# Performance work log

Hardware: AMD Instinct MI355X
Metric: run time of the kernel (lower is better)

## Reference

```python
import jax, jax.numpy as jnp
import numpy as np
from jax.ops import segment_sum, segment_max

N_NODES = 100000
N_EDGES = 1600000


def _glorot(key, shape):
    fan_in, fan_out = shape[0], shape[-1]
    lim = np.sqrt(6.0 / (fan_in + fan_out))
    return jax.random.uniform(key, shape, jnp.float32, -lim, lim)


def setup_inputs() -> dict:
    key = jax.random.key(0)
    ks = jax.random.split(key, 12)
    x = jax.random.normal(ks[0], (N_NODES, 7), jnp.float32)
    edge_index = jax.random.randint(ks[1], (2, N_EDGES), 0, N_NODES, jnp.int64)
    return {
        "x": x,
        "edge_index": edge_index,
        # GCNConv(7, 32)
        "W1": _glorot(ks[2], (7, 32)), "b1": jnp.zeros((32,), jnp.float32),
        # GATConv(32, 64), heads=1
        "W2": _glorot(ks[3], (32, 64)), "a_src2": _glorot(ks[4], (64, 1))[:, 0],
        "a_dst2": _glorot(ks[5], (64, 1))[:, 0], "b2": jnp.zeros((64,), jnp.float32),
        # GCNConv(64, 128)
        "W3": _glorot(ks[6], (64, 128)), "b3": jnp.zeros((128,), jnp.float32),
        # GATConv(128, 2), heads=1
        "W4": _glorot(ks[7], (128, 2)), "a_src4": _glorot(ks[8], (2, 1))[:, 0],
        "a_dst4": _glorot(ks[9], (2, 1))[:, 0], "b4": jnp.zeros((2,), jnp.float32),
    }


def _gcn_conv(x, src, dst, W, b):
    # x' = W x; symmetric normalization with self-loops already in (src, dst)
    h = x @ W
    deg = segment_sum(jnp.ones_like(dst, dtype=h.dtype), dst, num_segments=N_NODES)
    dinv = jnp.where(deg > 0, jax.lax.rsqrt(deg), 0.0)
    norm = dinv[src] * dinv[dst]            # [E]
    msg = norm[:, None] * h[src]            # [E, C]
    return segment_sum(msg, dst, num_segments=N_NODES) + b


def _gat_conv(x, src, dst, W, a_src, a_dst, b, slope=0.2):
    h = x @ W                               # [N, C]
    alpha_src = h @ a_src                   # [N]
    alpha_dst = h @ a_dst                   # [N]
    e = alpha_src[src] + alpha_dst[dst]     # [E]
    e = jnp.where(e > 0, e, slope * e)      # leaky_relu
    # numerically-stable softmax over edges grouped by destination node
    m = segment_max(e, dst, num_segments=N_NODES)
    ex = jnp.exp(e - m[dst])
    denom = segment_sum(ex, dst, num_segments=N_NODES)
    w = ex / (denom[dst] + 1e-16)           # [E]
    out = segment_sum(w[:, None] * h[src], dst, num_segments=N_NODES)
    return out + b


def reference(x, edge_index, W1, b1, W2, a_src2, a_dst2, b2, W3, b3, W4, a_src4, a_dst4, b4):
    # add self-loops once (PyG does it per layer; identical edge set each time)
    loop = jnp.arange(N_NODES, dtype=edge_index.dtype)
    src = jnp.concatenate([edge_index[0], loop])
    dst = jnp.concatenate([edge_index[1], loop])

    h = _gcn_conv(x, src, dst, W1, b1)
    h = jax.nn.relu(h)
    h = _gat_conv(h, src, dst, W2, a_src2, a_dst2, b2)
    h = jax.nn.relu(h)
    h = _gcn_conv(h, src, dst, W3, b3)
    h = jax.nn.relu(h)
    h = _gat_conv(h, src, dst, W4, a_src4, a_dst4, b4)
    return jax.nn.log_softmax(h, axis=1)
```

## Files before the change

### kernel.cpp

```cpp
#include <hip/hip_runtime.h>
#include <hip/hip_bf16.h>

#define NN 100000
#define NE 1600000
#define NT (NN + NE)
#define NBKT 256
#define BSZ 391
#define BCAP 10240

typedef unsigned int u32;
typedef unsigned short u16;

static __device__ __forceinline__ int clampN(int s) {
    return ((unsigned)s < (unsigned)NN) ? s : 0;
}
static __device__ __forceinline__ int ld_src(const int* ei, int is32, int e) {
    return is32 ? ei[e] : ei[2 * e];
}
static __device__ __forceinline__ int ld_dst(const int* ei, int is32, int e) {
    return is32 ? ei[NE + e] : ei[2 * NE + 2 * e];
}
static __device__ __forceinline__ float2 b2x2(u32 u) {
    float2 r;
    r.x = __uint_as_float((u & 0xffffu) << 16);
    r.y = __uint_as_float(u & 0xffff0000u);
    return r;
}
static __device__ __forceinline__ u16 f2bs(float f) {
    union { __hip_bfloat16 b; u16 u; } cv;
    cv.b = __float2bfloat16(f);
    return cv.u;
}
static __device__ __forceinline__ u32 pack2(float x, float y) {
    return ((u32)f2bs(y) << 16) | (u32)f2bs(x);
}
static __device__ __forceinline__ float lrelu_c(float e) {
    e = (e > 0.f) ? e : 0.2f * e;
    return fminf(e, 60.f);
}

#define FMA4(acc, s, v) { acc.x += (s)*(v).x; acc.y += (s)*(v).y; \
                          acc.z += (s)*(v).z; acc.w += (s)*(v).w; }


__global__ void __launch_bounds__(256) k_init(const float* __restrict__ W2,
                                              const float* __restrict__ a2s,
                                              const float* __restrict__ a2d,
                                              const int* __restrict__ ei,
                                              float* __restrict__ va2,
                                              float* __restrict__ vd2,
                                              int* __restrict__ flag,
                                              int* __restrict__ gcur) {
    if (blockIdx.x == 0) {
        if (threadIdx.x == 0) flag[0] = 0;
        __syncthreads();
        int nz = 0;
        for (int i = threadIdx.x; i < 4096; i += 256) nz |= ei[2 * i + 1];
        if (nz) atomicOr(flag, 1);
        if (threadIdx.x < NBKT) gcur[threadIdx.x] = 0;
    } else if (threadIdx.x < 64) {
        int t = threadIdx.x;
        if (t < 32) {
            float a = 0.f;
            for (int c = 0; c < 64; c++) a += W2[t * 64 + c] * a2s[c];
            va2[t] = a;
        } else {
            int k = t - 32;
            float a = 0.f;
            for (int c = 0; c < 64; c++) a += W2[k * 64 + c] * a2d[c];
            vd2[k] = a;
        }
    }
}


__global__ void __launch_bounds__(256) k_binA(const int* __restrict__ ei,
                                              const int* __restrict__ flag,
                                              int* __restrict__ gcur,
                                              u32* __restrict__ staging) {
    __shared__ int hist[NBKT];
    __shared__ int gbase[NBKT];
    __shared__ int cnt2[NBKT];
    int tid = threadIdx.x;
    if (tid < NBKT) hist[tid] = 0;
    __syncthreads();

    int base = blockIdx.x * 4096;
    int is32 = flag[0];
    int d[16], s[16];
    #pragma unroll
    for (int i = 0; i < 16; i++) {
        int e = base + i * 256 + tid;
        d[i] = -1;
        if (e < NE) {
            int dd = ld_dst(ei, is32, e);
            if ((unsigned)dd < (unsigned)NN) { d[i] = dd; s[i] = clampN(ld_src(ei, is32, e)); }
        } else if (e < NT) {
            d[i] = e - NE; s[i] = e - NE;
        }
        if (d[i] >= 0) atomicAdd(&hist[d[i] / BSZ], 1);
    }
    __syncthreads();
    if (tid < NBKT) {
        int c = hist[tid];
        gbase[tid] = c ? atomicAdd(&gcur[tid], c) : 0;
        cnt2[tid] = 0;
    }
    __syncthreads();
    #pragma unroll
    for (int i = 0; i < 16; i++) {
        if (d[i] >= 0) {
            int b = d[i] / BSZ;
            int pos = gbase[b] + atomicAdd(&cnt2[b], 1);
            if (pos < BCAP)
                staging[(size_t)b * BCAP + pos] =
                    ((unsigned)(d[i] - b * BSZ) << 17) | (unsigned)s[i];
        }
    }
}

__global__ void __launch_bounds__(256) k_histscan(const u32* __restrict__ staging,
                                                  const int* __restrict__ gcur,
                                                  const float* __restrict__ x,
                                                  u32* __restrict__ xpb,
                                                  int* __restrict__ rowptr,
                                                  int* __restrict__ deg,
                                                  int* __restrict__ part) {
    __shared__ int h[512];
    __shared__ int sm[256];
    int b = blockIdx.x, tid = threadIdx.x;
    h[tid] = 0; h[tid + 256] = 0;
    __syncthreads();
    int cnt = min(gcur[b], BCAP);
    const u32* st = staging + (size_t)b * BCAP;
    for (int i = tid; i < cnt; i += 256)
        atomicAdd(&h[st[i] >> 17], 1);
    __syncthreads();
    int h0 = h[2 * tid], h1 = h[2 * tid + 1];
    int pair = h0 + h1;
    sm[tid] = pair;
    __syncthreads();
    for (int off = 1; off < 256; off <<= 1) {
        int t = (tid >= off) ? sm[tid - off] : 0;
        __syncthreads();
        sm[tid] += t;
        __syncthreads();
    }
    int excl = sm[tid] - pair;
    int g0 = b * BSZ + 2 * tid;
    if (2 * tid < BSZ && g0 < NN) { rowptr[g0] = excl; deg[g0] = h0; }
    int g1 = g0 + 1;
    if (2 * tid + 1 < BSZ && g1 < NN) { rowptr[g1] = excl + h0; deg[g1] = h1; }
    if (tid == 255) part[b] = sm[255];

    for (int i = b * 256 + tid; i < NN * 4; i += NBKT * 256) {
        int n = i >> 2, c2 = i & 3;
        float f0 = x[n * 7 + 2 * c2];
        float f1 = (2 * c2 + 1 < 7) ? x[n * 7 + 2 * c2 + 1] : 0.f;
        xpb[i] = pack2(f0, f1);
    }
}

__global__ void __launch_bounds__(256) k_scat(const u32* __restrict__ staging,
                                              const int* __restrict__ gcur,
                                              const int* __restrict__ part,
                                              int* __restrict__ rowptr,
                                              const int* __restrict__ deg,
                                              float* __restrict__ dinv,
                                              int* __restrict__ col) {
    __shared__ int sm[256];
    __shared__ int cur[BSZ];
    int b = blockIdx.x, tid = threadIdx.x;
    int v = part[tid];
    sm[tid] = v;
    __syncthreads();
    for (int off = 1; off < 256; off <<= 1) {
        int t = (tid >= off) ? sm[tid - off] : 0;
        __syncthreads();
        sm[tid] += t;
        __syncthreads();
    }
    int pb = (b > 0) ? sm[b - 1] : 0;
    if (b == 0 && tid == 0) rowptr[NN] = NT;
    for (int l = tid; l < BSZ; l += 256) {
        int g = b * BSZ + l;
        if (g < NN) {
            int r = rowptr[g] + pb;
            rowptr[g] = r;
            cur[l] = r;
            int d = deg[g];
            dinv[g] = rsqrtf((float)(d > 0 ? d : 1));
        } else cur[l] = 0;
    }
    __syncthreads();
    int cnt = min(gcur[b], BCAP);
    const u32* st = staging + (size_t)b * BCAP;
    for (int i = tid; i < cnt; i += 256) {
        u32 w = st[i];
        int l = w >> 17;
        int s = w & 0x1FFFF;
        int p = atomicAdd(&cur[l], 1);
        if ((unsigned)p < (unsigned)NT) col[p] = s;
    }
}


__global__ void __launch_bounds__(256) k_l1(const u32* __restrict__ xpb,
                                            const int* __restrict__ rowptr,
                                            const int* __restrict__ col,
                                            const float* __restrict__ dinv,
                                            const float* __restrict__ W1,
                                            const float* __restrict__ b1,
                                            const float* __restrict__ va2,
                                            const float* __restrict__ vd2,
                                            u32* __restrict__ O1b,
                                            float* __restrict__ as_,
                                            float* __restrict__ ad_) {
    __shared__ float sW1[7 * 32];
    __shared__ float sb1[32], sva[32], svd[32];
    __shared__ float sT1[64 * 8];
    if (threadIdx.x < 224) sW1[threadIdx.x] = W1[threadIdx.x];
    else {
        int c = threadIdx.x - 224;
        sb1[c] = b1[c]; sva[c] = va2[c]; svd[c] = vd2[c];
    }
    __syncthreads();

    int node_l = threadIdx.x >> 2;
    int lane = threadIdx.x & 3;
    int slot = lane >> 1;
    int ck = lane & 1;
    int n = blockIdx.x * 64 + node_l;
    if (n >= NN) return;
    {
        int beg = rowptr[n], end = rowptr[n + 1];
        float a0 = 0.f, a1 = 0.f, a2 = 0.f, a3 = 0.f;
        #pragma unroll 2
        for (int e = beg + slot; e < end; e += 2) {
            int s = clampN(col[e]);
            float w = dinv[s];
            uint2 u = *(const uint2*)(xpb + (size_t)s * 4 + ck * 2);
            float2 f0 = b2x2(u.x), f1 = b2x2(u.y);
            a0 += w * f0.x; a1 += w * f0.y; a2 += w * f1.x; a3 += w * f1.y;
        }
        a0 += __shfl_xor(a0, 2, 4); a1 += __shfl_xor(a1, 2, 4);
        a2 += __shfl_xor(a2, 2, 4); a3 += __shfl_xor(a3, 2, 4);
        if (slot == 0) {
            float dn = dinv[n];
            float4 o = {a0 * dn, a1 * dn, a2 * dn, a3 * dn};
            *(float4*)&sT1[node_l * 8 + ck * 4] = o;
        }
    }
    __builtin_amdgcn_wave_barrier();
    int c8 = lane * 8;
    float4 aA = {0,0,0,0}, aB = {0,0,0,0};
    #pragma unroll
    for (int k = 0; k < 7; k++) {
        float t = sT1[node_l * 8 + k];
        float4 wva = *(const float4*)&sW1[k * 32 + c8];
        float4 wvb = *(const float4*)&sW1[k * 32 + c8 + 4];
        FMA4(aA, t, wva);
        FMA4(aB, t, wvb);
    }
    float o0 = fmaxf(aA.x + sb1[c8], 0.f);
    float o1 = fmaxf(aA.y + sb1[c8 + 1], 0.f);
    float o2 = fmaxf(aA.z + sb1[c8 + 2], 0.f);
    float o3 = fmaxf(aA.w + sb1[c8 + 3], 0.f);
    float o4 = fmaxf(aB.x + sb1[c8 + 4], 0.f);
    float o5 = fmaxf(aB.y + sb1[c8 + 5], 0.f);
    float o6 = fmaxf(aB.z + sb1[c8 + 6], 0.f);
    float o7 = fmaxf(aB.w + sb1[c8 + 7], 0.f);
    uint4 pk = {pack2(o0, o1), pack2(o2, o3), pack2(o4, o5), pack2(o6, o7)};
    *(uint4*)(O1b + (size_t)n * 16 + lane * 4) = pk;
    float vs = o0 * sva[c8] + o1 * sva[c8 + 1] + o2 * sva[c8 + 2] + o3 * sva[c8 + 3]
             + o4 * sva[c8 + 4] + o5 * sva[c8 + 5] + o6 * sva[c8 + 6] + o7 * sva[c8 + 7];
    float vd = o0 * svd[c8] + o1 * svd[c8 + 1] + o2 * svd[c8 + 2] + o3 * svd[c8 + 3]
             + o4 * svd[c8 + 4] + o5 * svd[c8 + 5] + o6 * svd[c8 + 6] + o7 * svd[c8 + 7];
    vs += __shfl_xor(vs, 1, 4); vs += __shfl_xor(vs, 2, 4);
    vd += __shfl_xor(vd, 1, 4); vd += __shfl_xor(vd, 2, 4);
    if (lane == 0) { as_[n] = vs; ad_[n] = vd; }
}


__global__ void __launch_bounds__(256) k_l2(const u32* __restrict__ O1b,
                                            const float* __restrict__ as_,
                                            const float* __restrict__ ad_,
                                            const int* __restrict__ rowptr,
                                            const int* __restrict__ col,
                                            const float* __restrict__ W2,
                                            const float* __restrict__ b2,
                                            const float* __restrict__ dinv,
                                            u32* __restrict__ O2b) {
    __shared__ float sW2[32 * 64];
    __shared__ float sT2[32 * 36];
    __shared__ float sb2[64];
    {
        const float4* g = (const float4*)W2;
        float4* s4 = (float4*)sW2;
        s4[threadIdx.x] = g[threadIdx.x];
        s4[threadIdx.x + 256] = g[threadIdx.x + 256];
    }
    if (threadIdx.x < 64) sb2[threadIdx.x] = b2[threadIdx.x];
    __syncthreads();

    int node_l = threadIdx.x >> 3;
    int l8 = threadIdx.x & 7;
    int slot = l8 >> 2;
    int ck = l8 & 3;
    int n = blockIdx.x * 32 + node_l;
    {
        int beg = rowptr[n], end = rowptr[n + 1];
        float adn = ad_[n];
        float den = 0.f;
        float a0=0.f,a1=0.f,a2=0.f,a3=0.f,a4=0.f,a5=0.f,a6=0.f,a7=0.f;
        #pragma unroll 2
        for (int e = beg + slot; e < end; e += 2) {
            int s = clampN(col[e]);
            float p = __expf(lrelu_c(as_[s] + adn));
            den += p;
            uint4 w = *(const uint4*)(O1b + (size_t)s * 16 + ck * 4);
            float2 f0 = b2x2(w.x), f1 = b2x2(w.y), f2 = b2x2(w.z), f3 = b2x2(w.w);
            a0 += p * f0.x; a1 += p * f0.y; a2 += p * f1.x; a3 += p * f1.y;
            a4 += p * f2.x; a5 += p * f2.y; a6 += p * f3.x; a7 += p * f3.y;
        }
        den += __shfl_xor(den, 4, 8);
        a0 += __shfl_xor(a0, 4, 8); a1 += __shfl_xor(a1, 4, 8);
        a2 += __shfl_xor(a2, 4, 8); a3 += __shfl_xor(a3, 4, 8);
        a4 += __shfl_xor(a4, 4, 8); a5 += __shfl_xor(a5, 4, 8);
        a6 += __shfl_xor(a6, 4, 8); a7 += __shfl_xor(a7, 4, 8);
        if (slot == 0) {
            float inv = 1.0f / (den + 1e-16f);
            float4 oA = {a0 * inv, a1 * inv, a2 * inv, a3 * inv};
            float4 oB = {a4 * inv, a5 * inv, a6 * inv, a7 * inv};
            float* dst = &sT2[node_l * 36 + ck * 8];
            *(float4*)dst = oA;
            *(float4*)(dst + 4) = oB;
        }
    }
    __builtin_amdgcn_wave_barrier();

    int grp = threadIdx.x >> 4;
    int l = threadIdx.x & 15;
    int c4 = l * 4;
    int lbase = grp * 2;

    float4 acc0 = {0,0,0,0}, acc1 = {0,0,0,0};
    #pragma unroll
    for (int k4 = 0; k4 < 8; k4++) {
        float4 t0 = *(const float4*)&sT2[(lbase + 0) * 36 + 4 * k4];
        float4 t1 = *(const float4*)&sT2[(lbase + 1) * 36 + 4 * k4];
        #pragma unroll
        for (int j = 0; j < 4; j++) {
            float4 wv = *(const float4*)&sW2[(4 * k4 + j) * 64 + c4];
            FMA4(acc0, ((const float*)&t0)[j], wv);
            FMA4(acc1, ((const float*)&t1)[j], wv);
        }
    }
    float4 bb = *(const float4*)&sb2[c4];
    int n0 = blockIdx.x * 32 + lbase;
    float d0 = dinv[n0], d1 = dinv[n0 + 1];
    {
        float o0 = fmaxf(acc0.x + bb.x, 0.f) * d0;
        float o1 = fmaxf(acc0.y + bb.y, 0.f) * d0;
        float o2 = fmaxf(acc0.z + bb.z, 0.f) * d0;
        float o3 = fmaxf(acc0.w + bb.w, 0.f) * d0;
        uint2 pk = {pack2(o0, o1), pack2(o2, o3)};
        *(uint2*)(O2b + (size_t)n0 * 32 + l * 2) = pk;
    }
    {
        float o0 = fmaxf(acc1.x + bb.x, 0.f) * d1;
        float o1 = fmaxf(acc1.y + bb.y, 0.f) * d1;
        float o2 = fmaxf(acc1.z + bb.z, 0.f) * d1;
        float o3 = fmaxf(acc1.w + bb.w, 0.f) * d1;
        uint2 pk = {pack2(o0, o1), pack2(o2, o3)};
        *(uint2*)(O2b + (size_t)(n0 + 1) * 32 + l * 2) = pk;
    }
}


__global__ void __launch_bounds__(512, 8) k_l3(const u32* __restrict__ O2b,
                                               const int* __restrict__ rowptr,
                                               const int* __restrict__ col,
                                               const float* __restrict__ dinv,
                                               const float* __restrict__ W3,
                                               const float* __restrict__ b3,
                                               const float* __restrict__ W4,
                                               const float* __restrict__ av4s,
                                               const float* __restrict__ av4d,
                                               float4* __restrict__ h4as,
                                               float* __restrict__ ad_) {
    __shared__ float sW3[64 * 128];
    __shared__ float sW4[128 * 2];
    __shared__ float sb3[128];

    {
        const float4* g = (const float4*)W3;
        float4* s4 = (float4*)sW3;
        #pragma unroll
        for (int i = 0; i < 4; i++) s4[threadIdx.x + 512 * i] = g[threadIdx.x + 512 * i];
    }
    if (threadIdx.x < 128) {
        sb3[threadIdx.x] = b3[threadIdx.x];
        sW4[2 * threadIdx.x] = W4[2 * threadIdx.x];
        sW4[2 * threadIdx.x + 1] = W4[2 * threadIdx.x + 1];
    }
    __syncthreads();

    int l = threadIdx.x & 63;
    int cl = l & 7;
    int row = (threadIdx.x >> 6) * 8 + (l >> 3);
    int n = blockIdx.x * 64 + row;
    if (n >= NN) return;

    float4 accA = {0,0,0,0}, accB = {0,0,0,0};
    {
        int beg = rowptr[n], end = rowptr[n + 1];
        #pragma unroll 4
        for (int e = beg; e < end; e++) {
            int s = clampN(col[e]);
            uint4 wd = *(const uint4*)(O2b + (size_t)s * 32 + cl * 4);
            float2 f0 = b2x2(wd.x), f1 = b2x2(wd.y), f2 = b2x2(wd.z), f3 = b2x2(wd.w);
            accA.x += f0.x; accA.y += f0.y; accA.z += f1.x; accA.w += f1.y;
            accB.x += f2.x; accB.y += f2.y; accB.z += f3.x; accB.w += f3.y;
        }
        float dn = dinv[n];
        accA.x *= dn; accA.y *= dn; accA.z *= dn; accA.w *= dn;
        accB.x *= dn; accB.y *= dn; accB.z *= dn; accB.w *= dn;
    }

    float4 acc0 = {0,0,0,0}, acc1 = {0,0,0,0}, acc2 = {0,0,0,0}, acc3 = {0,0,0,0};
    #pragma unroll
    for (int k4 = 0; k4 < 16; k4++) {
        int src = k4 >> 1;
        float t0, t1, t2, t3;
        if (k4 & 1) {
            t0 = __shfl(accB.x, src, 8); t1 = __shfl(accB.y, src, 8);
            t2 = __shfl(accB.z, src, 8); t3 = __shfl(accB.w, src, 8);
        } else {
            t0 = __shfl(accA.x, src, 8); t1 = __shfl(accA.y, src, 8);
            t2 = __shfl(accA.z, src, 8); t3 = __shfl(accA.w, src, 8);
        }
        #pragma unroll
        for (int j = 0; j < 4; j++) {
            float tj = (j == 0) ? t0 : (j == 1) ? t1 : (j == 2) ? t2 : t3;
            const float* wr = &sW3[(4 * k4 + j) * 128 + 4 * cl];
            float4 w0 = *(const float4*)&wr[0];
            float4 w1 = *(const float4*)&wr[32];
            float4 w2 = *(const float4*)&wr[64];
            float4 w3v = *(const float4*)&wr[96];
            FMA4(acc0, tj, w0);
            FMA4(acc1, tj, w1);
            FMA4(acc2, tj, w2);
            FMA4(acc3, tj, w3v);
        }
    }

    float av4s0 = av4s[0], av4s1 = av4s[1];
    float av4d0 = av4d[0], av4d1 = av4d[1];
    float p0 = 0.f, p1 = 0.f;
    #pragma unroll
    for (int q = 0; q < 4; q++) {
        float4 a = (q == 0) ? acc0 : (q == 1) ? acc1 : (q == 2) ? acc2 : acc3;
        int c = 4 * cl + 32 * q;
        float4 bb = *(const float4*)&sb3[c];
        a.x = fmaxf(a.x + bb.x, 0.f);
        a.y = fmaxf(a.y + bb.y, 0.f);
        a.z = fmaxf(a.z + bb.z, 0.f);
        a.w = fmaxf(a.w + bb.w, 0.f);
        p0 += a.x * sW4[2 * c]     + a.y * sW4[2 * (c + 1)]
            + a.z * sW4[2 * (c + 2)] + a.w * sW4[2 * (c + 3)];
        p1 += a.x * sW4[2 * c + 1]     + a.y * sW4[2 * (c + 1) + 1]
            + a.z * sW4[2 * (c + 2) + 1] + a.w * sW4[2 * (c + 3) + 1];
    }
    p0 += __shfl_xor(p0, 1, 8); p0 += __shfl_xor(p0, 2, 8); p0 += __shfl_xor(p0, 4, 8);
    p1 += __shfl_xor(p1, 1, 8); p1 += __shfl_xor(p1, 2, 8); p1 += __shfl_xor(p1, 4, 8);
    if (cl == 0) {
        float asv = p0 * av4s0 + p1 * av4s1;
        float4 pk = {p0, p1, asv, 0.f};
        h4as[n] = pk;
        ad_[n] = p0 * av4d0 + p1 * av4d1;
    }
}


__global__ void k_final(const float4* __restrict__ h4as,
                        const float* __restrict__ ad_, const int* __restrict__ rowptr,
                        const int* __restrict__ col, const float* __restrict__ b,
                        float* __restrict__ out) {
    int gid = blockIdx.x * 256 + threadIdx.x;
    int n = gid >> 2;
    if (n >= NN) return;
    int lsub = gid & 3;
    int beg = rowptr[n], end = rowptr[n + 1];
    float adn = ad_[n];
    float den = 0.f, a0 = 0.f, a1 = 0.f;
    for (int e = beg + lsub; e < end; e += 4) {
        int s = clampN(col[e]);
        float4 h = h4as[s];
        float p = __expf(lrelu_c(h.z + adn));
        den += p;
        a0 += p * h.x;
        a1 += p * h.y;
    }
    den += __shfl_xor(den, 1, 4); den += __shfl_xor(den, 2, 4);
    a0  += __shfl_xor(a0, 1, 4);  a0  += __shfl_xor(a0, 2, 4);
    a1  += __shfl_xor(a1, 1, 4);  a1  += __shfl_xor(a1, 2, 4);
    if (lsub == 0) {
        float inv = 1.0f / (den + 1e-16f);
        float v0 = a0 * inv + b[0];
        float v1 = a1 * inv + b[1];
        float mx = fmaxf(v0, v1);
        float lse = mx + logf(__expf(v0 - mx) + __expf(v1 - mx));
        float2 o = {v0 - lse, v1 - lse};
        *(float2*)(out + n * 2) = o;
    }
}

__global__ void k_sentinel(float* __restrict__ out, float v) {
    int i = blockIdx.x * 256 + threadIdx.x;
    if (i < NN * 2) out[i] = v;
}


extern "C" void kernel_launch(void* const* d_in, const int* in_sizes, int n_in,
                              void* d_out, int out_size, void* d_ws, size_t ws_size,
                              hipStream_t stream) {
    const float* x    = (const float*)d_in[0];
    const int* ei     = (const int*)d_in[1];
    const float* W1   = (const float*)d_in[2];
    const float* b1   = (const float*)d_in[3];
    const float* W2   = (const float*)d_in[4];
    const float* a2s  = (const float*)d_in[5];
    const float* a2d  = (const float*)d_in[6];
    const float* b2   = (const float*)d_in[7];
    const float* W3   = (const float*)d_in[8];
    const float* b3   = (const float*)d_in[9];
    const float* W4   = (const float*)d_in[10];
    const float* a4s  = (const float*)d_in[11];
    const float* a4d  = (const float*)d_in[12];
    const float* b4   = (const float*)d_in[13];
    float* out = (float*)d_out;

    char* base = (char*)d_ws;
    size_t off = 0;
    auto alloc = [&](size_t bytes) {
        char* q = base + off;
        off += (bytes + 255) & ~(size_t)255;
        return q;
    };
    u32* xpb     = (u32*)alloc((size_t)NN * 4 * 4);
    u32* O1b     = (u32*)alloc((size_t)NN * 16 * 4);
    u32* O2b     = (u32*)alloc((size_t)NN * 32 * 4);
    u32* staging = (u32*)alloc((size_t)NBKT * BCAP * 4);
    int* col     = (int*)alloc((size_t)NT * 4);
    int* rowptr  = (int*)alloc((size_t)(NN + 1) * 4);
    int* deg     = (int*)alloc((size_t)NN * 4);
    float* dinv  = (float*)alloc((size_t)NN * 4);
    float* as_   = (float*)alloc((size_t)NN * 4);
    float* ad_   = (float*)alloc((size_t)NN * 4);
    float4* h4as = (float4*)alloc((size_t)NN * 16);
    int* part    = (int*)alloc(512 * 4);
    int* flag    = (int*)alloc(256);
    int* gcur    = (int*)alloc(NBKT * 4);
    float* va2   = (float*)alloc(32 * 4);
    float* vd2   = (float*)alloc(32 * 4);

    float code = 0.f;
    if (off > ws_size)            code = 1000.f + (float)(ws_size >> 20);
    else if (n_in != 14)          code = 2000.f + 10.f * (float)n_in;
    else if (out_size != NN * 2)  code = 3400.f;
    if (code != 0.f) {
        k_sentinel<<<(NN * 2 + 255) / 256, 256, 0, stream>>>(out, code);
        return;
    }

    const int NTILE = (NT + 4095) / 4096;

    k_init<<<2, 256, 0, stream>>>(W2, a2s, a2d, ei, va2, vd2, flag, gcur);
    k_binA<<<NTILE, 256, 0, stream>>>(ei, flag, gcur, staging);
    k_histscan<<<NBKT, 256, 0, stream>>>(staging, gcur, x, xpb, rowptr, deg, part);
    k_scat<<<NBKT, 256, 0, stream>>>(staging, gcur, part, rowptr, deg, dinv, col);

    k_l1<<<(NN + 63) / 64, 256, 0, stream>>>(xpb, rowptr, col, dinv,
                                             W1, b1, va2, vd2, O1b, as_, ad_);
    k_l2<<<NN / 32, 256, 0, stream>>>(O1b, as_, ad_, rowptr, col,
                                      W2, b2, dinv, O2b);
    k_l3<<<(NN + 63) / 64, 512, 0, stream>>>(O2b, rowptr, col, dinv,
                                             W3, b3, W4, a4s, a4d, h4as, ad_);
    k_final<<<NN * 4 / 256 + 1, 256, 0, stream>>>(h4as, ad_, rowptr, col, b4, out);
}
```

Baseline: 258.4 us.

## Stage layer-3 aggregates in LDS and double k_l3 block size

In k_l3 each 8-lane row group now writes its aggregated 64-wide feature row into a padded shared-memory tile and reads it back as float4 for the 64x128 matmul, where it previously broadcast values with __shfl. Blocks grow from 512 to 1024 threads, covering 128 nodes each, so the 32KB W3 copy in LDS is loaded half as often per node. The edge loader in k_binA also reads int64 indices as int2 low words. This adds about 35KB of LDS per block, which together with 1024-thread blocks may cap residency, and it relies on a wave barrier because each row group sits inside a single wave.

```diff
diff --git a/kernel.cpp b/kernel.cpp
--- a/kernel.cpp
+++ b/kernel.cpp
@@ -13,12 +13,6 @@
 
 static __device__ __forceinline__ int clampN(int s) {
     return ((unsigned)s < (unsigned)NN) ? s : 0;
-}
-static __device__ __forceinline__ int ld_src(const int* ei, int is32, int e) {
-    return is32 ? ei[e] : ei[2 * e];
-}
-static __device__ __forceinline__ int ld_dst(const int* ei, int is32, int e) {
-    return is32 ? ei[NE + e] : ei[2 * NE + 2 * e];
 }
 static __device__ __forceinline__ float2 b2x2(u32 u) {
     float2 r;
@@ -93,8 +87,15 @@
         int e = base + i * 256 + tid;
         d[i] = -1;
         if (e < NE) {
-            int dd = ld_dst(ei, is32, e);
-            if ((unsigned)dd < (unsigned)NN) { d[i] = dd; s[i] = clampN(ld_src(ei, is32, e)); }
+            int dd, ss;
+            if (is32) {
+                dd = ei[NE + e];
+                ss = ei[e];
+            } else {
+                dd = ((const int2*)ei)[NE + e].x;
+                ss = ((const int2*)ei)[e].x;
+            }
+            if ((unsigned)dd < (unsigned)NN) { d[i] = dd; s[i] = clampN(ss); }
         } else if (e < NT) {
             d[i] = e - NE; s[i] = e - NE;
         }
@@ -378,18 +379,19 @@
 }
 
 
-__global__ void __launch_bounds__(512, 8) k_l3(const u32* __restrict__ O2b,
-                                               const int* __restrict__ rowptr,
-                                               const int* __restrict__ col,
-                                               const float* __restrict__ dinv,
-                                               const float* __restrict__ W3,
-                                               const float* __restrict__ b3,
-                                               const float* __restrict__ W4,
-                                               const float* __restrict__ av4s,
-                                               const float* __restrict__ av4d,
-                                               float4* __restrict__ h4as,
-                                               float* __restrict__ ad_) {
+__global__ void __launch_bounds__(1024, 8) k_l3(const u32* __restrict__ O2b,
+                                                const int* __restrict__ rowptr,
+                                                const int* __restrict__ col,
+                                                const float* __restrict__ dinv,
+                                                const float* __restrict__ W3,
+                                                const float* __restrict__ b3,
+                                                const float* __restrict__ W4,
+                                                const float* __restrict__ av4s,
+                                                const float* __restrict__ av4d,
+                                                float4* __restrict__ h4as,
+                                                float* __restrict__ ad_) {
     __shared__ float sW3[64 * 128];
+    __shared__ float sT3[128 * 68];
     __shared__ float sW4[128 * 2];
     __shared__ float sb3[128];
 
@@ -397,7 +399,7 @@
         const float4* g = (const float4*)W3;
         float4* s4 = (float4*)sW3;
         #pragma unroll
-        for (int i = 0; i < 4; i++) s4[threadIdx.x + 512 * i] = g[threadIdx.x + 512 * i];
+        for (int i = 0; i < 2; i++) s4[threadIdx.x + 1024 * i] = g[threadIdx.x + 1024 * i];
     }
     if (threadIdx.x < 128) {
         sb3[threadIdx.x] = b3[threadIdx.x];
@@ -406,15 +408,16 @@
     }
     __syncthreads();
 
+    int w = threadIdx.x >> 6;
     int l = threadIdx.x & 63;
+    int row = w * 8 + (l >> 3);
     int cl = l & 7;
-    int row = (threadIdx.x >> 6) * 8 + (l >> 3);
-    int n = blockIdx.x * 64 + row;
+    int n = blockIdx.x * 128 + row;
     if (n >= NN) return;
 
-    float4 accA = {0,0,0,0}, accB = {0,0,0,0};
     {
         int beg = rowptr[n], end = rowptr[n + 1];
+        float4 accA = {0,0,0,0}, accB = {0,0,0,0};
         #pragma unroll 4
         for (int e = beg; e < end; e++) {
             int s = clampN(col[e]);
@@ -426,23 +429,20 @@
         float dn = dinv[n];
         accA.x *= dn; accA.y *= dn; accA.z *= dn; accA.w *= dn;
         accB.x *= dn; accB.y *= dn; accB.z *= dn; accB.w *= dn;
-    }
-
+        float* dst = &sT3[row * 68 + cl * 8];
+        *(float4*)dst = accA;
+        *(float4*)(dst + 4) = accB;
+    }
+    __builtin_amdgcn_wave_barrier();
+
+    const float* trow = &sT3[row * 68];
     float4 acc0 = {0,0,0,0}, acc1 = {0,0,0,0}, acc2 = {0,0,0,0}, acc3 = {0,0,0,0};
-    #pragma unroll
+    #pragma unroll 4
     for (int k4 = 0; k4 < 16; k4++) {
-        int src = k4 >> 1;
-        float t0, t1, t2, t3;
-        if (k4 & 1) {
-            t0 = __shfl(accB.x, src, 8); t1 = __shfl(accB.y, src, 8);
-            t2 = __shfl(accB.z, src, 8); t3 = __shfl(accB.w, src, 8);
-        } else {
-            t0 = __shfl(accA.x, src, 8); t1 = __shfl(accA.y, src, 8);
-            t2 = __shfl(accA.z, src, 8); t3 = __shfl(accA.w, src, 8);
-        }
+        float4 t4 = *(const float4*)&trow[k4 * 4];
         #pragma unroll
         for (int j = 0; j < 4; j++) {
-            float tj = (j == 0) ? t0 : (j == 1) ? t1 : (j == 2) ? t2 : t3;
+            float tj = ((const float*)&t4)[j];
             const float* wr = &sW3[(4 * k4 + j) * 128 + 4 * cl];
             float4 w0 = *(const float4*)&wr[0];
             float4 w1 = *(const float4*)&wr[32];
@@ -585,7 +585,7 @@
                                              W1, b1, va2, vd2, O1b, as_, ad_);
     k_l2<<<NN / 32, 256, 0, stream>>>(O1b, as_, ad_, rowptr, col,
                                       W2, b2, dinv, O2b);
-    k_l3<<<(NN + 63) / 64, 512, 0, stream>>>(O2b, rowptr, col, dinv,
-                                             W3, b3, W4, a4s, a4d, h4as, ad_);
+    k_l3<<<(NN + 127) / 128, 1024, 0, stream>>>(O2b, rowptr, col, dinv,
+                                                W3, b3, W4, a4s, a4d, h4as, ad_);
     k_final<<<NN * 4 / 256 + 1, 256, 0, stream>>>(h4as, ad_, rowptr, col, b4, out);
 }
```

Result: no change. 257.8 us (-0.2%).
